# Performance work log

Hardware: AMD Instinct MI355X
Metric: run time of the kernel (lower is better)

The kernel has to match this reference:

```python
import jax, jax.numpy as jnp
import numpy as np

B, D, M = 16384, 512, 16

def setup_inputs() -> dict:
    key = jax.random.key(0)
    k1, k2, k3 = jax.random.split(key, 3)
    z = jax.random.normal(k1, (B, D), dtype=jnp.float32)
    # Psi: n_dynamics small [D,D] operators (orthogonal-init in torch; random here)
    Psi = jax.random.normal(k2, (M, D, D), dtype=jnp.float32) * 0.001
    gate_tokens = jax.random.normal(k3, (M, D), dtype=jnp.float32) * (1.0 / np.sqrt(D))
    t = jnp.zeros((1,), dtype=jnp.float32)  # unused by forward, kept for signature parity
    return {"t": t, "z": z, "Psi": Psi, "gate_tokens": gate_tokens}

def reference(t, z, Psi, gate_tokens):
    # scores[b,m,e] = (z @ Psi_m)[b,e]  -- batched small GEMM over M dynamics
    scores = jnp.einsum('bd,mde->bme', z, Psi)
    # gate logits and sparse-soft gates: relu(2*sigmoid(logits) - 1)
    logits = jnp.einsum('bme,me->bm', scores, gate_tokens)
    gates = jax.nn.relu(2.0 * jax.nn.sigmoid(logits) - 1.0)
    # dz[b,e] = sum_m gates[b,m] * scores[b,m,e]
    dz = jnp.einsum('bm,bme->be', gates, scores)
    return dz
```

## Files before the change

kernel.cpp:

```cpp
#include <hip/hip_runtime.h>
#include <hip/hip_bf16.h>

#define B_N 16384
#define D_N 512
#define M_N 16

typedef __attribute__((ext_vector_type(4))) float  f32x4;
typedef __attribute__((ext_vector_type(2))) float  f32x2;
typedef __attribute__((ext_vector_type(8))) short  s16x8;
typedef __attribute__((ext_vector_type(4))) unsigned short u16x4;

__device__ __forceinline__ short bf16_of(float f) {
  union { float f; unsigned u; } v; v.f = f;
  unsigned r = v.u + 0x7fffu + ((v.u >> 16) & 1u);
  return (short)(r >> 16);
}
__device__ __forceinline__ float f32_of_bf16(unsigned short u) {
  union { unsigned u; float f; } v; v.u = ((unsigned)u) << 16; return v.f;
}
__device__ __forceinline__ void gload_lds16(const void* g, void* l) {
  __builtin_amdgcn_global_load_lds(
      (const __attribute__((address_space(1))) unsigned*)g,
      (__attribute__((address_space(3))) unsigned*)l, 16, 0, 0);
}

#define MFMA_ACC(d, x, y) d = __builtin_amdgcn_mfma_f32_16x16x32_bf16(x, y, d, 0, 0, 0)
#define MFMA_Z(d, x, y)   d = __builtin_amdgcn_mfma_f32_16x16x32_bf16(x, y, FZERO, 0, 0, 0)

__global__ void k_trw(const float* __restrict__ Psi, const float* __restrict__ gt,
                      short* __restrict__ Psib, float* __restrict__ wT) {
  int m = blockIdx.y, d0 = blockIdx.x << 6;
  __shared__ float tile[64][65];
  __shared__ float gs[D_N];
  int t = threadIdx.x;
  for (int i = t; i < D_N; i += 256) gs[i] = gt[m * D_N + i];
  int r = t >> 2, q = t & 3;
  float wacc = 0.f;
  const float* src = Psi + (size_t)m * D_N * D_N;
  short* dst = Psib + (size_t)m * D_N * D_N;
  for (int e0 = 0; e0 < D_N; e0 += 64) {
    __syncthreads();
    #pragma unroll
    for (int j = 0; j < 4; ++j) {
      int idx = t + (j << 8);
      int rr = idx >> 4, c4 = idx & 15;
      *(f32x4*)&tile[rr][c4 * 4] = *(const f32x4*)(src + (size_t)(d0 + rr) * D_N + e0 + c4 * 4);
    }
    __syncthreads();
    #pragma unroll
    for (int k = 0; k < 16; ++k) wacc += tile[r][q * 16 + k] * gs[e0 + q * 16 + k];
    #pragma unroll
    for (int it = 0; it < 2; ++it) {
      int idx = t + (it << 8);
      int el = idx >> 3, jb = idx & 7;
      int e = e0 + el;
      s16x8 o;
      #pragma unroll
      for (int k = 0; k < 8; ++k) o[k] = bf16_of(tile[jb * 8 + k][el]);
      int db = jb ^ (e & 7);
      *(s16x8*)(dst + (size_t)e * D_N + d0 + db * 8) = o;
    }
  }
  wacc += __shfl_xor(wacc, 1);
  wacc += __shfl_xor(wacc, 2);
  if (q == 0) wT[(d0 + r) * M_N + m] = wacc;
}

__global__ void k_gz(const float* __restrict__ z, const float* __restrict__ wT,
                     short* __restrict__ zb, unsigned short* __restrict__ gatesb) {
  __shared__ float zs[16][D_N];
  int t = threadIdx.x;
  size_t b0 = (size_t)blockIdx.x * 16;
  #pragma unroll
  for (int j = 0; j < 8; ++j) {
    int idx = t + (j << 8);
    int r = idx >> 7, c4 = idx & 127;
    *(f32x4*)&zs[r][c4 * 4] = *(const f32x4*)(z + (b0 + r) * D_N + c4 * 4);
  }
  __syncthreads();
  int r = t >> 4, m = t & 15;
  float s0 = 0.f, s1 = 0.f, s2 = 0.f, s3 = 0.f;
  #pragma unroll 4
  for (int e = 0; e < D_N; e += 4) {
    s0 += zs[r][e + 0] * wT[(e + 0) * M_N + m];
    s1 += zs[r][e + 1] * wT[(e + 1) * M_N + m];
    s2 += zs[r][e + 2] * wT[(e + 2) * M_N + m];
    s3 += zs[r][e + 3] * wT[(e + 3) * M_N + m];
  }
  float s = (s0 + s1) + (s2 + s3);
  float sig = 1.f / (1.f + expf(-s));
  gatesb[(b0 + r) * M_N + m] = (unsigned short)bf16_of(fmaxf(2.f * sig - 1.f, 0.f));
  #pragma unroll
  for (int j = 0; j < 4; ++j) {
    int idx = t + (j << 8);
    int rr = idx >> 6, blk = idx & 63;
    int chunk = blk >> 3, ib = blk & 7;
    int sb = ib ^ (rr & 7);
    const float* sp = &zs[rr][chunk * 64 + sb * 8];
    s16x8 o;
    #pragma unroll
    for (int k = 0; k < 8; ++k) o[k] = bf16_of(sp[k]);
    *(s16x8*)(zb + (b0 + rr) * D_N + blk * 8) = o;
  }
}

__global__ __launch_bounds__(512, 4) void k_gemm(
    const char* __restrict__ zb, const unsigned short* __restrict__ gatesb,
    const char* __restrict__ pb, float* __restrict__ dz) {
  __shared__ __align__(128) char smem[73728];
  float* glf = (float*)(smem + 65536);

  const int tid = threadIdx.x;
  const int lane = tid & 63;
  const int wid = tid >> 6;
  const int wr = wid >> 1;
  const int wc = wid & 1;
  const int bid = blockIdx.x;
  const int xcd = bid & 7;
  const int g8 = bid >> 3;
  const int bcol = g8 & 3;
  const int brow = xcd * 16 + (g8 >> 2);

  {
    int row = tid >> 2, g4 = tid & 3;
    u16x4 gv = *(const u16x4*)(gatesb + ((size_t)(brow * 128 + row) << 4) + (g4 << 2));
    #pragma unroll
    for (int k = 0; k < 4; ++k)
      glf[(g4 * 4 + k) * 128 + row] = f32_of_bf16(gv[k]);
  }

  const int rsub = lane >> 3, cbyte = (lane & 7) << 4;

  auto stageA = [&](int ab, int dc) {
    #pragma unroll
    for (int j = 0; j < 2; ++j) {
      const char* g = zb + (((size_t)(brow * 128 + wid * 8 + j * 64 + rsub)) << 10)
                      + (dc << 7) + cbyte;
      gload_lds16(g, smem + ab * 16384 + (wid << 10) + (j << 13));
    }
  };
  auto stageB = [&](int m, int dc, int qb) {
    #pragma unroll
    for (int j = 0; j < 2; ++j) {
      const char* g = pb + (((size_t)(m * 512 + bcol * 128 + wid * 8 + j * 64 + rsub)) << 10)
                      + (dc << 7) + cbyte;
      gload_lds16(g, smem + 32768 + qb * 16384 + (wid << 10) + (j << 13));
    }
  };

  const int lrow = lane & 15;
  const int kq16 = (((lane >> 4) << 4)) ^ ((lrow & 7) << 4);
  const int offY = ((wr * 32 + lrow) << 7) + kq16;
  const int offX = ((wc * 64 + lrow) << 7) + kq16;
  const int grow = wr * 32 + lrow;

  f32x4 acc[4][2] = {};
  f32x4 accm[4][2];
  s16x8 areg[2][2];
  const f32x4 FZERO = {0.f, 0.f, 0.f, 0.f};

  stageA(0, 0);
  stageB(0, 0, 0);
  asm volatile("s_waitcnt vmcnt(0) lgkmcnt(0)" ::: "memory");
  __builtin_amdgcn_s_barrier();

  #pragma unroll 1
  for (int s = 0; s < 128; ++s) {
    const int m = s & 15, dc = s >> 4;

    if (s < 127) stageB((s + 1) & 15, (s + 1) >> 4, (s + 1) & 1);
    if (m == 14 && dc < 7) stageA((dc & 1) ^ 1, dc + 1);

    if (m == 0) {
      const char* abase = smem + (dc & 1) * 16384;
      #pragma unroll
      for (int j = 0; j < 2; ++j) {
        areg[j][0] = *(const s16x8*)(abase + (offY + j * 2048));
        areg[j][1] = *(const s16x8*)(abase + ((offY + j * 2048) ^ 64));
      }
    }
    float g0 = glf[m * 128 + grow];
    float g1 = glf[m * 128 + grow + 16];

    const char* bbase = smem + 32768 + (s & 1) * 16384;
    {
      s16x8 b0 = *(const s16x8*)(bbase + (offX));
      s16x8 b1 = *(const s16x8*)(bbase + (offX + 2048));
      s16x8 b2 = *(const s16x8*)(bbase + (offX + 4096));
      s16x8 b3 = *(const s16x8*)(bbase + (offX + 6144));
      __builtin_amdgcn_s_setprio(1);
      MFMA_Z(accm[0][0], b0, areg[0][0]); MFMA_Z(accm[0][1], b0, areg[1][0]);
      MFMA_Z(accm[1][0], b1, areg[0][0]); MFMA_Z(accm[1][1], b1, areg[1][0]);
      MFMA_Z(accm[2][0], b2, areg[0][0]); MFMA_Z(accm[2][1], b2, areg[1][0]);
      MFMA_Z(accm[3][0], b3, areg[0][0]); MFMA_Z(accm[3][1], b3, areg[1][0]);
      __builtin_amdgcn_s_setprio(0);
    }
    {
      s16x8 b0 = *(const s16x8*)(bbase + (offX ^ 64));
      s16x8 b1 = *(const s16x8*)(bbase + ((offX + 2048) ^ 64));
      s16x8 b2 = *(const s16x8*)(bbase + ((offX + 4096) ^ 64));
      s16x8 b3 = *(const s16x8*)(bbase + ((offX + 6144) ^ 64));
      __builtin_amdgcn_s_setprio(1);
      MFMA_ACC(accm[0][0], b0, areg[0][1]); MFMA_ACC(accm[0][1], b0, areg[1][1]);
      MFMA_ACC(accm[1][0], b1, areg[0][1]); MFMA_ACC(accm[1][1], b1, areg[1][1]);
      MFMA_ACC(accm[2][0], b2, areg[0][1]); MFMA_ACC(accm[2][1], b2, areg[1][1]);
      MFMA_ACC(accm[3][0], b3, areg[0][1]); MFMA_ACC(accm[3][1], b3, areg[1][1]);
      __builtin_amdgcn_s_setprio(0);
    }
    #pragma unroll
    for (int i = 0; i < 4; ++i) {
      f32x2 ga = {g0, g0}, gb = {g1, g1};
      f32x2* a0 = (f32x2*)&acc[i][0];
      f32x2* a1 = (f32x2*)&acc[i][1];
      const f32x2* m0p = (const f32x2*)&accm[i][0];
      const f32x2* m1p = (const f32x2*)&accm[i][1];
      a0[0] += ga * m0p[0]; a0[1] += ga * m0p[1];
      a1[0] += gb * m1p[0]; a1[1] += gb * m1p[1];
    }

    asm volatile("s_waitcnt vmcnt(0)" ::: "memory");
    __builtin_amdgcn_s_barrier();
  }

  #pragma unroll
  for (int i = 0; i < 4; ++i) {
    int e = bcol * 128 + wc * 64 + i * 16 + ((lane >> 4) << 2);
    #pragma unroll
    for (int j = 0; j < 2; ++j) {
      size_t b = (size_t)brow * 128 + wr * 32 + j * 16 + lrow;
      *(f32x4*)(dz + b * D_N + e) = acc[i][j];
    }
  }
}

extern "C" void kernel_launch(void* const* d_in, const int* in_sizes, int n_in,
                              void* d_out, int out_size, void* d_ws, size_t ws_size,
                              hipStream_t stream) {
  const float* z   = (const float*)d_in[1];
  const float* Psi = (const float*)d_in[2];
  const float* gt  = (const float*)d_in[3];
  float* dz = (float*)d_out;

  float* wT = (float*)d_ws;
  unsigned short* gatesb = (unsigned short*)((char*)d_ws + 32768);
  short* Psib = (short*)((char*)d_ws + 32768 + 524288);
  short* zb16 = Psib + (size_t)M_N * D_N * D_N;

  k_trw <<<dim3(8, M_N), dim3(256), 0, stream>>>(Psi, gt, Psib, wT);
  k_gz  <<<dim3(B_N / 16), dim3(256), 0, stream>>>(z, wT, zb16, gatesb);
  k_gemm<<<dim3(512), dim3(512), 0, stream>>>((const char*)zb16, gatesb,
                                              (const char*)Psib, dz);
}
```

Measured before the change: 161.3 us.

## Switch GEMM to 32x32x16 MFMA with pre-tiled layouts and triple-buffered Psi staging

The main GEMM now uses 32x32x16 bf16 MFMA tiles instead of 16x16x32. The preprocessing kernels write z and Psi in an MFMA-friendly tiled order, so each wave's global-to-LDS copies are contiguous, unswizzled 16-byte loads. Psi staging goes from double to triple buffering with a prefetch distance of two and graded vmcnt waits, and z is staged once per k-chunk into a single buffer. This is meant to cut LDS read instructions and MFMA issue count per step and to hide load latency better. In exchange it uses larger per-lane accumulators (two f32x16) and relies on delicate wait counting and a single z buffer being reused safely.

```diff
diff --git a/kernel.cpp b/kernel.cpp
--- a/kernel.cpp
+++ b/kernel.cpp
@@ -5,10 +5,10 @@
 #define D_N 512
 #define M_N 16
 
-typedef __attribute__((ext_vector_type(4))) float  f32x4;
-typedef __attribute__((ext_vector_type(2))) float  f32x2;
-typedef __attribute__((ext_vector_type(8))) short  s16x8;
-typedef __attribute__((ext_vector_type(4))) unsigned short u16x4;
+typedef __attribute__((ext_vector_type(4)))  float f32x4;
+typedef __attribute__((ext_vector_type(16))) float f32x16;
+typedef __attribute__((ext_vector_type(8)))  short s16x8;
+typedef __attribute__((ext_vector_type(4)))  unsigned short u16x4;
 
 __device__ __forceinline__ short bf16_of(float f) {
   union { float f; unsigned u; } v; v.f = f;
@@ -24,12 +24,9 @@
       (__attribute__((address_space(3))) unsigned*)l, 16, 0, 0);
 }
 
-#define MFMA_ACC(d, x, y) d = __builtin_amdgcn_mfma_f32_16x16x32_bf16(x, y, d, 0, 0, 0)
-#define MFMA_Z(d, x, y)   d = __builtin_amdgcn_mfma_f32_16x16x32_bf16(x, y, FZERO, 0, 0, 0)
-
 __global__ void k_trw(const float* __restrict__ Psi, const float* __restrict__ gt,
                       short* __restrict__ Psib, float* __restrict__ wT) {
-  int m = blockIdx.y, d0 = blockIdx.x << 6;
+  int m = blockIdx.y, bx = blockIdx.x, d0 = bx << 6;
   __shared__ float tile[64][65];
   __shared__ float gs[D_N];
   int t = threadIdx.x;
@@ -37,7 +34,6 @@
   int r = t >> 2, q = t & 3;
   float wacc = 0.f;
   const float* src = Psi + (size_t)m * D_N * D_N;
-  short* dst = Psib + (size_t)m * D_N * D_N;
   for (int e0 = 0; e0 < D_N; e0 += 64) {
     __syncthreads();
     #pragma unroll
@@ -57,8 +53,9 @@
       s16x8 o;
       #pragma unroll
       for (int k = 0; k < 8; ++k) o[k] = bf16_of(tile[jb * 8 + k][el]);
-      int db = jb ^ (e & 7);
-      *(s16x8*)(dst + (size_t)e * D_N + d0 + db * 8) = o;
+      size_t off = ((size_t)((((m << 2) + (e >> 7)) << 3) | bx) << 13)
+                 + (jb << 10) + ((e & 127) << 3);
+      *(s16x8*)(Psib + off) = o;
     }
   }
   wacc += __shfl_xor(wacc, 1);
@@ -92,15 +89,14 @@
   gatesb[(b0 + r) * M_N + m] = (unsigned short)bf16_of(fmaxf(2.f * sig - 1.f, 0.f));
   #pragma unroll
   for (int j = 0; j < 4; ++j) {
-    int idx = t + (j << 8);
-    int rr = idx >> 6, blk = idx & 63;
-    int chunk = blk >> 3, ib = blk & 7;
-    int sb = ib ^ (rr & 7);
-    const float* sp = &zs[rr][chunk * 64 + sb * 8];
+    int u = t + (j << 8);
+    int rr = u & 15, c = u >> 4;
     s16x8 o;
     #pragma unroll
-    for (int k = 0; k < 8; ++k) o[k] = bf16_of(sp[k]);
-    *(s16x8*)(zb + (b0 + rr) * D_N + blk * 8) = o;
+    for (int k = 0; k < 8; ++k) o[k] = bf16_of(zs[rr][(c << 3) + k]);
+    size_t off = ((size_t)(b0 >> 7) << 17) + ((size_t)(c >> 3) << 14)
+               + ((c & 7) << 11) + ((((int)(b0 & 127)) + rr) << 4);
+    *(s16x8*)((char*)zb + off) = o;
   }
 }
 
@@ -129,106 +125,111 @@
       glf[(g4 * 4 + k) * 128 + row] = f32_of_bf16(gv[k]);
   }
 
-  const int rsub = lane >> 3, cbyte = (lane & 7) << 4;
-
-  auto stageA = [&](int ab, int dc) {
-    #pragma unroll
-    for (int j = 0; j < 2; ++j) {
-      const char* g = zb + (((size_t)(brow * 128 + wid * 8 + j * 64 + rsub)) << 10)
-                      + (dc << 7) + cbyte;
-      gload_lds16(g, smem + ab * 16384 + (wid << 10) + (j << 13));
-    }
+  const int lnoff = (wid << 11) + (lane << 4);
+  const char* zsrc = zb + (size_t)brow * 131072 + lnoff;
+  const char* bsrc = pb + ((size_t)bcol << 17) + lnoff;
+
+  auto stageA = [&](int dc) {
+    const char* g = zsrc + (dc << 14);
+    char* l = smem + (wid << 11);
+    gload_lds16(g, l);
+    gload_lds16(g + 1024, l + 1024);
   };
-  auto stageB = [&](int m, int dc, int qb) {
-    #pragma unroll
-    for (int j = 0; j < 2; ++j) {
-      const char* g = pb + (((size_t)(m * 512 + bcol * 128 + wid * 8 + j * 64 + rsub)) << 10)
-                      + (dc << 7) + cbyte;
-      gload_lds16(g, smem + 32768 + qb * 16384 + (wid << 10) + (j << 13));
-    }
+  auto stageB = [&](int m, int dc, int q) {
+    const char* g = bsrc + ((size_t)m << 19) + (dc << 14);
+    char* l = smem + 16384 + (q << 14) + (wid << 11);
+    gload_lds16(g, l);
+    gload_lds16(g + 1024, l + 1024);
   };
 
-  const int lrow = lane & 15;
-  const int kq16 = (((lane >> 4) << 4)) ^ ((lrow & 7) << 4);
-  const int offY = ((wr * 32 + lrow) << 7) + kq16;
-  const int offX = ((wc * 64 + lrow) << 7) + kq16;
-  const int grow = wr * 32 + lrow;
-
-  f32x4 acc[4][2] = {};
-  f32x4 accm[4][2];
-  s16x8 areg[2][2];
-  const f32x4 FZERO = {0.f, 0.f, 0.f, 0.f};
-
-  stageA(0, 0);
+  const int lhalf = lane >> 5;
+  const int lrow32 = lane & 31;
+  const int zoff = (lhalf << 11) + ((wr * 32 + lrow32) << 4);
+  const int poff = (lhalf << 11) + ((wc * 64 + lrow32) << 4);
+
+  f32x16 acc0 = {}, acc1 = {};
+  s16x8 zf[4];
+  const f32x16 FZ = {};
+
+  stageA(0);
   stageB(0, 0, 0);
+  stageB(1, 0, 1);
   asm volatile("s_waitcnt vmcnt(0) lgkmcnt(0)" ::: "memory");
   __builtin_amdgcn_s_barrier();
 
+  int q = 0;
   #pragma unroll 1
   for (int s = 0; s < 128; ++s) {
     const int m = s & 15, dc = s >> 4;
-
-    if (s < 127) stageB((s + 1) & 15, (s + 1) >> 4, (s + 1) & 1);
-    if (m == 14 && dc < 7) stageA((dc & 1) ^ 1, dc + 1);
+    int q2 = q + 2; if (q2 >= 3) q2 -= 3;
+
+    if (s + 2 < 128) stageB((s + 2) & 15, (s + 2) >> 4, q2);
+    const bool aw = (m == 1) && (dc < 7);
+    if (aw) stageA(dc + 1);
 
     if (m == 0) {
-      const char* abase = smem + (dc & 1) * 16384;
+      zf[0] = *(const s16x8*)(smem + zoff);
+      zf[1] = *(const s16x8*)(smem + zoff + 4096);
+      zf[2] = *(const s16x8*)(smem + zoff + 8192);
+      zf[3] = *(const s16x8*)(smem + zoff + 12288);
+    }
+    float g = glf[(m << 7) + wr * 32 + lrow32];
+    const char* bb = smem + 16384 + (q << 14);
+
+    {
+      s16x8 p0 = *(const s16x8*)(bb + poff);
+      s16x8 p1 = *(const s16x8*)(bb + poff + 4096);
+      s16x8 p2 = *(const s16x8*)(bb + poff + 8192);
+      s16x8 p3 = *(const s16x8*)(bb + poff + 12288);
+      __builtin_amdgcn_s_setprio(1);
+      f32x16 accm = __builtin_amdgcn_mfma_f32_32x32x16_bf16(p0, zf[0], FZ, 0, 0, 0);
+      accm = __builtin_amdgcn_mfma_f32_32x32x16_bf16(p1, zf[1], accm, 0, 0, 0);
+      accm = __builtin_amdgcn_mfma_f32_32x32x16_bf16(p2, zf[2], accm, 0, 0, 0);
+      accm = __builtin_amdgcn_mfma_f32_32x32x16_bf16(p3, zf[3], accm, 0, 0, 0);
+      __builtin_amdgcn_s_setprio(0);
       #pragma unroll
-      for (int j = 0; j < 2; ++j) {
-        areg[j][0] = *(const s16x8*)(abase + (offY + j * 2048));
-        areg[j][1] = *(const s16x8*)(abase + ((offY + j * 2048) ^ 64));
-      }
-    }
-    float g0 = glf[m * 128 + grow];
-    float g1 = glf[m * 128 + grow + 16];
-
-    const char* bbase = smem + 32768 + (s & 1) * 16384;
+      for (int i = 0; i < 16; ++i) acc0[i] = fmaf(g, accm[i], acc0[i]);
+    }
     {
-      s16x8 b0 = *(const s16x8*)(bbase + (offX));
-      s16x8 b1 = *(const s16x8*)(bbase + (offX + 2048));
-      s16x8 b2 = *(const s16x8*)(bbase + (offX + 4096));
-      s16x8 b3 = *(const s16x8*)(bbase + (offX + 6144));
+      s16x8 p0 = *(const s16x8*)(bb + poff + 512);
+      s16x8 p1 = *(const s16x8*)(bb + poff + 512 + 4096);
+      s16x8 p2 = *(const s16x8*)(bb + poff + 512 + 8192);
+      s16x8 p3 = *(const s16x8*)(bb + poff + 512 + 12288);
       __builtin_amdgcn_s_setprio(1);
-      MFMA_Z(accm[0][0], b0, areg[0][0]); MFMA_Z(accm[0][1], b0, areg[1][0]);
-      MFMA_Z(accm[1][0], b1, areg[0][0]); MFMA_Z(accm[1][1], b1, areg[1][0]);
-      MFMA_Z(accm[2][0], b2, areg[0][0]); MFMA_Z(accm[2][1], b2, areg[1][0]);
-      MFMA_Z(accm[3][0], b3, areg[0][0]); MFMA_Z(accm[3][1], b3, areg[1][0]);
+      f32x16 accm = __builtin_amdgcn_mfma_f32_32x32x16_bf16(p0, zf[0], FZ, 0, 0, 0);
+      accm = __builtin_amdgcn_mfma_f32_32x32x16_bf16(p1, zf[1], accm, 0, 0, 0);
+      accm = __builtin_amdgcn_mfma_f32_32x32x16_bf16(p2, zf[2], accm, 0, 0, 0);
+      accm = __builtin_amdgcn_mfma_f32_32x32x16_bf16(p3, zf[3], accm, 0, 0, 0);
       __builtin_amdgcn_s_setprio(0);
-    }
-    {
-      s16x8 b0 = *(const s16x8*)(bbase + (offX ^ 64));
-      s16x8 b1 = *(const s16x8*)(bbase + ((offX + 2048) ^ 64));
-      s16x8 b2 = *(const s16x8*)(bbase + ((offX + 4096) ^ 64));
-      s16x8 b3 = *(const s16x8*)(bbase + ((offX + 6144) ^ 64));
-      __builtin_amdgcn_s_setprio(1);
-      MFMA_ACC(accm[0][0], b0, areg[0][1]); MFMA_ACC(accm[0][1], b0, areg[1][1]);
-      MFMA_ACC(accm[1][0], b1, areg[0][1]); MFMA_ACC(accm[1][1], b1, areg[1][1]);
-      MFMA_ACC(accm[2][0], b2, areg[0][1]); MFMA_ACC(accm[2][1], b2, areg[1][1]);
-      MFMA_ACC(accm[3][0], b3, areg[0][1]); MFMA_ACC(accm[3][1], b3, areg[1][1]);
-      __builtin_amdgcn_s_setprio(0);
-    }
-    #pragma unroll
-    for (int i = 0; i < 4; ++i) {
-      f32x2 ga = {g0, g0}, gb = {g1, g1};
-      f32x2* a0 = (f32x2*)&acc[i][0];
-      f32x2* a1 = (f32x2*)&acc[i][1];
-      const f32x2* m0p = (const f32x2*)&accm[i][0];
-      const f32x2* m1p = (const f32x2*)&accm[i][1];
-      a0[0] += ga * m0p[0]; a0[1] += ga * m0p[1];
-      a1[0] += gb * m1p[0]; a1[1] += gb * m1p[1];
-    }
-
-    asm volatile("s_waitcnt vmcnt(0)" ::: "memory");
-    __builtin_amdgcn_s_barrier();
-  }
-
-  #pragma unroll
-  for (int i = 0; i < 4; ++i) {
-    int e = bcol * 128 + wc * 64 + i * 16 + ((lane >> 4) << 2);
-    #pragma unroll
-    for (int j = 0; j < 2; ++j) {
-      size_t b = (size_t)brow * 128 + wr * 32 + j * 16 + lrow;
-      *(f32x4*)(dz + b * D_N + e) = acc[i][j];
+      #pragma unroll
+      for (int i = 0; i < 16; ++i) acc1[i] = fmaf(g, accm[i], acc1[i]);
+    }
+
+    if (s < 127) {
+      if (s >= 126)
+        asm volatile("s_waitcnt vmcnt(0)" ::: "memory");
+      else if ((m == 1 || m == 2) && dc < 7)
+        asm volatile("s_waitcnt vmcnt(4)" ::: "memory");
+      else
+        asm volatile("s_waitcnt vmcnt(2)" ::: "memory");
+      __builtin_amdgcn_s_barrier();
+    }
+    q = (q + 1 == 3) ? 0 : q + 1;
+  }
+
+  {
+    size_t bglob = (size_t)brow * 128 + wr * 32 + lrow32;
+    int ebase = bcol * 128 + wc * 64 + (lhalf << 2);
+    float* out = dz + bglob * D_N + ebase;
+    #pragma unroll
+    for (int qq = 0; qq < 4; ++qq) {
+      f32x4 v = {acc0[4 * qq + 0], acc0[4 * qq + 1], acc0[4 * qq + 2], acc0[4 * qq + 3]};
+      *(f32x4*)(out + qq * 8) = v;
+    }
+    #pragma unroll
+    for (int qq = 0; qq < 4; ++qq) {
+      f32x4 v = {acc1[4 * qq + 0], acc1[4 * qq + 1], acc1[4 * qq + 2], acc1[4 * qq + 3]};
+      *(f32x4*)(out + 32 + qq * 8) = v;
     }
   }
 }
```

Measured after the change: 187.8 us. 1.16x slower.

## Triple-buffer Psi tiles with prefetch distance two and single-buffer z tile

Applied to the files above, without the earlier changes.

Psi tiles now go into a three-slot ring buffer and are prefetched two steps ahead instead of one. The z tile drops to a single buffer, which is safe because its fragments sit in registers before the buffer is overwritten, so total LDS usage stays the same. The full vmcnt(0) drain each iteration becomes a partial wait (vmcnt 2 or 4), so later loads stay in flight across the barrier. This aims to hide global-to-LDS latency better, but relies on exact counting of outstanding loads for correctness.

```diff
diff --git a/kernel.cpp b/kernel.cpp
--- a/kernel.cpp
+++ b/kernel.cpp
@@ -131,12 +131,12 @@
 
   const int rsub = lane >> 3, cbyte = (lane & 7) << 4;
 
-  auto stageA = [&](int ab, int dc) {
+  auto stageA = [&](int dc) {
     #pragma unroll
     for (int j = 0; j < 2; ++j) {
       const char* g = zb + (((size_t)(brow * 128 + wid * 8 + j * 64 + rsub)) << 10)
                       + (dc << 7) + cbyte;
-      gload_lds16(g, smem + ab * 16384 + (wid << 10) + (j << 13));
+      gload_lds16(g, smem + (wid << 10) + (j << 13));
     }
   };
   auto stageB = [&](int m, int dc, int qb) {
@@ -144,7 +144,7 @@
     for (int j = 0; j < 2; ++j) {
       const char* g = pb + (((size_t)(m * 512 + bcol * 128 + wid * 8 + j * 64 + rsub)) << 10)
                       + (dc << 7) + cbyte;
-      gload_lds16(g, smem + 32768 + qb * 16384 + (wid << 10) + (j << 13));
+      gload_lds16(g, smem + 16384 + (qb << 14) + (wid << 10) + (j << 13));
     }
   };
 
@@ -159,52 +159,55 @@
   s16x8 areg[2][2];
   const f32x4 FZERO = {0.f, 0.f, 0.f, 0.f};
 
-  stageA(0, 0);
+  stageA(0);
   stageB(0, 0, 0);
+  stageB(1, 0, 1);
   asm volatile("s_waitcnt vmcnt(0) lgkmcnt(0)" ::: "memory");
   __builtin_amdgcn_s_barrier();
 
+  int q = 0;
   #pragma unroll 1
   for (int s = 0; s < 128; ++s) {
     const int m = s & 15, dc = s >> 4;
-
-    if (s < 127) stageB((s + 1) & 15, (s + 1) >> 4, (s + 1) & 1);
-    if (m == 14 && dc < 7) stageA((dc & 1) ^ 1, dc + 1);
+    int q2 = q + 2; if (q2 >= 3) q2 -= 3;
+
+    if (s + 2 < 128) stageB((s + 2) & 15, (s + 2) >> 4, q2);
+    const bool aw = (m == 14) && (dc < 7);
+    if (aw) stageA(dc + 1);
 
     if (m == 0) {
-      const char* abase = smem + (dc & 1) * 16384;
       #pragma unroll
       for (int j = 0; j < 2; ++j) {
-        areg[j][0] = *(const s16x8*)(abase + (offY + j * 2048));
-        areg[j][1] = *(const s16x8*)(abase + ((offY + j * 2048) ^ 64));
+        areg[j][0] = *(const s16x8*)(smem + (offY + j * 2048));
+        areg[j][1] = *(const s16x8*)(smem + ((offY + j * 2048) ^ 64));
       }
     }
-    float g0 = glf[m * 128 + grow];
-    float g1 = glf[m * 128 + grow + 16];
-
-    const char* bbase = smem + 32768 + (s & 1) * 16384;
+    float g0 = glf[(m << 7) + grow];
+    float g1 = glf[(m << 7) + grow + 16];
+
+    const char* bbase = smem + 16384 + (q << 14);
     {
-      s16x8 b0 = *(const s16x8*)(bbase + (offX));
-      s16x8 b1 = *(const s16x8*)(bbase + (offX + 2048));
-      s16x8 b2 = *(const s16x8*)(bbase + (offX + 4096));
-      s16x8 b3 = *(const s16x8*)(bbase + (offX + 6144));
+      s16x8 p0 = *(const s16x8*)(bbase + (offX));
+      s16x8 p1 = *(const s16x8*)(bbase + (offX + 2048));
+      s16x8 p2 = *(const s16x8*)(bbase + (offX + 4096));
+      s16x8 p3 = *(const s16x8*)(bbase + (offX + 6144));
       __builtin_amdgcn_s_setprio(1);
-      MFMA_Z(accm[0][0], b0, areg[0][0]); MFMA_Z(accm[0][1], b0, areg[1][0]);
-      MFMA_Z(accm[1][0], b1, areg[0][0]); MFMA_Z(accm[1][1], b1, areg[1][0]);
-      MFMA_Z(accm[2][0], b2, areg[0][0]); MFMA_Z(accm[2][1], b2, areg[1][0]);
-      MFMA_Z(accm[3][0], b3, areg[0][0]); MFMA_Z(accm[3][1], b3, areg[1][0]);
+      MFMA_Z(accm[0][0], p0, areg[0][0]); MFMA_Z(accm[0][1], p0, areg[1][0]);
+      MFMA_Z(accm[1][0], p1, areg[0][0]); MFMA_Z(accm[1][1], p1, areg[1][0]);
+      MFMA_Z(accm[2][0], p2, areg[0][0]); MFMA_Z(accm[2][1], p2, areg[1][0]);
+      MFMA_Z(accm[3][0], p3, areg[0][0]); MFMA_Z(accm[3][1], p3, areg[1][0]);
       __builtin_amdgcn_s_setprio(0);
     }
     {
-      s16x8 b0 = *(const s16x8*)(bbase + (offX ^ 64));
-      s16x8 b1 = *(const s16x8*)(bbase + ((offX + 2048) ^ 64));
-      s16x8 b2 = *(const s16x8*)(bbase + ((offX + 4096) ^ 64));
-      s16x8 b3 = *(const s16x8*)(bbase + ((offX + 6144) ^ 64));
+      s16x8 p0 = *(const s16x8*)(bbase + (offX ^ 64));
+      s16x8 p1 = *(const s16x8*)(bbase + ((offX + 2048) ^ 64));
+      s16x8 p2 = *(const s16x8*)(bbase + ((offX + 4096) ^ 64));
+      s16x8 p3 = *(const s16x8*)(bbase + ((offX + 6144) ^ 64));
       __builtin_amdgcn_s_setprio(1);
-      MFMA_ACC(accm[0][0], b0, areg[0][1]); MFMA_ACC(accm[0][1], b0, areg[1][1]);
-      MFMA_ACC(accm[1][0], b1, areg[0][1]); MFMA_ACC(accm[1][1], b1, areg[1][1]);
-      MFMA_ACC(accm[2][0], b2, areg[0][1]); MFMA_ACC(accm[2][1], b2, areg[1][1]);
-      MFMA_ACC(accm[3][0], b3, areg[0][1]); MFMA_ACC(accm[3][1], b3, areg[1][1]);
+      MFMA_ACC(accm[0][0], p0, areg[0][1]); MFMA_ACC(accm[0][1], p0, areg[1][1]);
+      MFMA_ACC(accm[1][0], p1, areg[0][1]); MFMA_ACC(accm[1][1], p1, areg[1][1]);
+      MFMA_ACC(accm[2][0], p2, areg[0][1]); MFMA_ACC(accm[2][1], p2, areg[1][1]);
+      MFMA_ACC(accm[3][0], p3, areg[0][1]); MFMA_ACC(accm[3][1], p3, areg[1][1]);
       __builtin_amdgcn_s_setprio(0);
     }
     #pragma unroll
@@ -218,8 +221,14 @@
       a1[0] += gb * m1p[0]; a1[1] += gb * m1p[1];
     }
 
-    asm volatile("s_waitcnt vmcnt(0)" ::: "memory");
-    __builtin_amdgcn_s_barrier();
+    if (aw)
+      asm volatile("s_waitcnt vmcnt(4)" ::: "memory");
+    else if (s >= 126)
+      asm volatile("s_waitcnt vmcnt(0)" ::: "memory");
+    else
+      asm volatile("s_waitcnt vmcnt(2)" ::: "memory");
+    if (s < 127) __builtin_amdgcn_s_barrier();
+    q = (q + 1 == 3) ? 0 : q + 1;
   }
 
   #pragma unroll
```

Measured after the change: 170.6 us. 5.8% more time.

## Split Psi transpose and gate-weight kernel to raise grid parallelism

Applied to the files above, without the earlier changes.

The fused transpose-plus-gate-vector kernel used only 128 blocks, each looping serially over eight 64-wide column tiles. It is split into two kernels: a row-dot kernel with 512 blocks computing w = Psi·gate_tokens through wave shuffles, and a transpose/bf16-cast kernel with 1024 blocks, one tile each. This aims to fill the GPU during preprocessing, at the cost of reading Psi twice and adding one more kernel launch.

```diff
diff --git a/kernel.cpp b/kernel.cpp
--- a/kernel.cpp
+++ b/kernel.cpp
@@ -27,43 +27,53 @@
 #define MFMA_ACC(d, x, y) d = __builtin_amdgcn_mfma_f32_16x16x32_bf16(x, y, d, 0, 0, 0)
 #define MFMA_Z(d, x, y)   d = __builtin_amdgcn_mfma_f32_16x16x32_bf16(x, y, FZERO, 0, 0, 0)
 
-__global__ void k_trw(const float* __restrict__ Psi, const float* __restrict__ gt,
-                      short* __restrict__ Psib, float* __restrict__ wT) {
-  int m = blockIdx.y, d0 = blockIdx.x << 6;
+__global__ void k_w(const float* __restrict__ Psi, const float* __restrict__ gt,
+                    float* __restrict__ wT) {
+  int m = blockIdx.x;
+  int d0 = blockIdx.y * 16;
+  __shared__ float g[D_N];
+  for (int i = threadIdx.x; i < D_N; i += 256) g[i] = gt[m * D_N + i];
+  __syncthreads();
+  int wave = threadIdx.x >> 6, lane = threadIdx.x & 63;
+  #pragma unroll
+  for (int d = d0 + wave; d < d0 + 16; d += 4) {
+    const float* row = Psi + ((size_t)m * D_N + d) * D_N;
+    const f32x4* r4 = (const f32x4*)(row + lane * 8);
+    const f32x4* g4 = (const f32x4*)(g + lane * 8);
+    f32x4 a0 = r4[0], a1 = r4[1];
+    f32x4 b0 = g4[0], b1 = g4[1];
+    float s = a0[0]*b0[0] + a0[1]*b0[1] + a0[2]*b0[2] + a0[3]*b0[3]
+            + a1[0]*b1[0] + a1[1]*b1[1] + a1[2]*b1[2] + a1[3]*b1[3];
+    #pragma unroll
+    for (int off = 32; off; off >>= 1) s += __shfl_down(s, off);
+    if (lane == 0) wT[d * M_N + m] = s;
+  }
+}
+
+__global__ void k_tr(const float* __restrict__ Psi, short* __restrict__ Psib) {
+  int m = blockIdx.z, d0 = blockIdx.x << 6, e0 = blockIdx.y << 6;
   __shared__ float tile[64][65];
-  __shared__ float gs[D_N];
   int t = threadIdx.x;
-  for (int i = t; i < D_N; i += 256) gs[i] = gt[m * D_N + i];
-  int r = t >> 2, q = t & 3;
-  float wacc = 0.f;
   const float* src = Psi + (size_t)m * D_N * D_N;
   short* dst = Psib + (size_t)m * D_N * D_N;
-  for (int e0 = 0; e0 < D_N; e0 += 64) {
-    __syncthreads();
-    #pragma unroll
-    for (int j = 0; j < 4; ++j) {
-      int idx = t + (j << 8);
-      int rr = idx >> 4, c4 = idx & 15;
-      *(f32x4*)&tile[rr][c4 * 4] = *(const f32x4*)(src + (size_t)(d0 + rr) * D_N + e0 + c4 * 4);
-    }
-    __syncthreads();
-    #pragma unroll
-    for (int k = 0; k < 16; ++k) wacc += tile[r][q * 16 + k] * gs[e0 + q * 16 + k];
-    #pragma unroll
-    for (int it = 0; it < 2; ++it) {
-      int idx = t + (it << 8);
-      int el = idx >> 3, jb = idx & 7;
-      int e = e0 + el;
-      s16x8 o;
-      #pragma unroll
-      for (int k = 0; k < 8; ++k) o[k] = bf16_of(tile[jb * 8 + k][el]);
-      int db = jb ^ (e & 7);
-      *(s16x8*)(dst + (size_t)e * D_N + d0 + db * 8) = o;
-    }
-  }
-  wacc += __shfl_xor(wacc, 1);
-  wacc += __shfl_xor(wacc, 2);
-  if (q == 0) wT[(d0 + r) * M_N + m] = wacc;
+  #pragma unroll
+  for (int j = 0; j < 4; ++j) {
+    int idx = t + (j << 8);
+    int rr = idx >> 4, c4 = idx & 15;
+    *(f32x4*)&tile[rr][c4 * 4] = *(const f32x4*)(src + (size_t)(d0 + rr) * D_N + e0 + c4 * 4);
+  }
+  __syncthreads();
+  #pragma unroll
+  for (int it = 0; it < 2; ++it) {
+    int idx = t + (it << 8);
+    int el = idx >> 3, jb = idx & 7;
+    int e = e0 + el;
+    s16x8 o;
+    #pragma unroll
+    for (int k = 0; k < 8; ++k) o[k] = bf16_of(tile[jb * 8 + k][el]);
+    int db = jb ^ (e & 7);
+    *(s16x8*)(dst + (size_t)e * D_N + d0 + db * 8) = o;
+  }
 }
 
 __global__ void k_gz(const float* __restrict__ z, const float* __restrict__ wT,
@@ -246,8 +256,9 @@
   short* Psib = (short*)((char*)d_ws + 32768 + 524288);
   short* zb16 = Psib + (size_t)M_N * D_N * D_N;
 
-  k_trw <<<dim3(8, M_N), dim3(256), 0, stream>>>(Psi, gt, Psib, wT);
-  k_gz  <<<dim3(B_N / 16), dim3(256), 0, stream>>>(z, wT, zb16, gatesb);
-  k_gemm<<<dim3(512), dim3(512), 0, stream>>>((const char*)zb16, gatesb,
-                                              (const char*)Psib, dz);
-}
+  k_w   <<<dim3(M_N, 32),   dim3(256), 0, stream>>>(Psi, gt, wT);
+  k_tr  <<<dim3(8, 8, M_N), dim3(256), 0, stream>>>(Psi, Psib);
+  k_gz  <<<dim3(B_N / 16),  dim3(256), 0, stream>>>(z, wT, zb16, gatesb);
+  k_gemm<<<dim3(512),       dim3(512), 0, stream>>>((const char*)zb16, gatesb,
+                                                    (const char*)Psib, dz);
+}
```

Result: no change. 159.0 us (-1.4%).
